# Optimization experiments

Hardware: AMD Instinct MI355X
Metric: run time of the kernel (lower is better)

Reference implementation:

```python
import jax, jax.numpy as jnp
import numpy as np

B, T = 8, 2048
DV, DA = 1024, 128          # visual / audio feature dims
D1, D2 = 512, 128           # conv1d channels
DH = D2 + DA + 1            # 257: lorentz dim after time-coord pad
DG = 128                    # per-branch GCN output dim (args.dim)
NEG = 0.01                  # LeakyReLU slope
K_CURV = 1.0
EPS = 1e-6


def leaky(x):
    return jnp.where(x >= 0, x, NEG * x)


def expmap0_lorentz(x):
    # x: [B,T,DH] with x[...,0] == 0 (tangent at origin), k = 1
    xs = x[..., 1:]
    n = jnp.sqrt(jnp.maximum(jnp.sum(xs * xs, -1, keepdims=True), 1e-12))
    return jnp.concatenate([jnp.cosh(n), jnp.sinh(n) / n * xs], axis=-1)


def lorentz_similarity(x):
    # xy_inner = -<x,x>_L  (negate time component of left factor, negate product)
    signs = jnp.concatenate([-jnp.ones((1,), x.dtype), jnp.ones((DH - 1,), x.dtype)])
    xy = -jnp.einsum('bid,bjd->bij', x * signs, x)          # [B,T,T]
    xy = jnp.maximum(xy, 1.0)                                # F.threshold(., 1, 1)
    d = (K_CURV ** 0.5) * jnp.log(xy + jnp.sqrt(xy * xy - 1.0 + 1e-7))
    return jnp.clip(d, EPS, 200.0)


def adj_fn(proj_x, seq_len):
    x2 = jnp.exp(-lorentz_similarity(proj_x))               # [B,T,T]
    pos = jnp.arange(T)
    row = pos[None, :, None] < seq_len[:, None, None]       # [B,T,1]
    col = pos[None, None, :] < seq_len[:, None, None]       # [B,1,T]
    thr = jnp.where(x2 > 0.8, x2, 0.0)                      # F.threshold(., 0.8, 0)
    logits = jnp.where(col, thr, -1e30)                     # softmax over valid cols
    p = jax.nn.softmax(logits, axis=-1)
    return p * (row & col)                                  # zero outside [:L,:L]


def clas_fn(logits, seq_len):
    # logits: [B,T]; per-sample top-k (k = L//16 + 1) mean, then sigmoid
    pos = jnp.arange(T)
    valid = pos[None, :] < seq_len[:, None]
    masked = jnp.where(valid, logits, -1e30)
    srt = -jnp.sort(-masked, axis=1)                         # descending
    k = seq_len // 16 + 1                                    # [B]
    kmask = pos[None, :] < k[:, None]
    mil = jnp.sum(srt * kmask, axis=1) / k.astype(logits.dtype)
    return jax.nn.sigmoid(mil)


def forward(inputs, seq_len, w1, b1, w2, b2, gw1, gw2, cls_w, cls_b):
    xv = inputs[:, :, :DV]
    xa = inputs[:, :, DV:]
    xv = leaky(jnp.einsum('btc,oc->bto', xv, w1) + b1)       # conv1d k=1
    xv = leaky(jnp.einsum('btc,oc->bto', xv, w2) + b2)
    x = jnp.concatenate([xv, xa], axis=-1)                   # [B,T,256]

    # DistanceAdj: exp(-|i-j| / e), shared across batch
    pos = jnp.arange(T, dtype=jnp.float32)
    disadj = jnp.exp(-jnp.abs(pos[:, None] - pos[None, :]) / jnp.exp(1.0))  # [T,T]

    # expm: pad time coord, lorentz expmap0
    proj_x = expmap0_lorentz(
        jnp.concatenate([jnp.zeros(x.shape[:-1] + (1,), x.dtype), x], axis=-1))  # [B,T,257]

    adj = adj_fn(proj_x, seq_len)                            # [B,T,T]

    x1 = leaky(jnp.einsum('bij,bjd->bid', adj, proj_x) @ gw1)        # HFSGCN stand-in
    x2 = leaky(jnp.einsum('ij,bjd->bid', disadj, proj_x) @ gw2)      # HTRGCN stand-in
    out_x = jnp.concatenate([x1, x2], axis=-1)               # [B,T,256]

    # HypClassifier: 2 + 2*<x, cls>_L + bias  (lorentz inner)
    signs = jnp.concatenate([-jnp.ones((1,), out_x.dtype), jnp.ones((2 * DG - 1,), out_x.dtype)])
    frame_prob = 2.0 + 2.0 * jnp.einsum('btd,cd->btc', out_x * signs, cls_w) + cls_b  # [B,T,1]

    mil_logits = clas_fn(frame_prob[..., 0], seq_len)        # [B]
    return mil_logits, frame_prob


def setup_inputs() -> dict:
    key = jax.random.key(0)
    ks = jax.random.split(key, 8)
    inputs = jax.random.normal(ks[0], (B, T, DV + DA), jnp.float32)
    seq_len = jax.random.randint(ks[1], (B,), T // 2, T + 1, jnp.int32)
    w1 = jax.random.normal(ks[2], (D1, DV), jnp.float32) / np.float32(np.sqrt(DV))
    b1 = jnp.zeros((D1,), jnp.float32)
    w2 = jax.random.normal(ks[3], (D2, D1), jnp.float32) / np.float32(np.sqrt(D1))
    b2 = jnp.zeros((D2,), jnp.float32)
    gw1 = jax.random.normal(ks[4], (DH, DG), jnp.float32) / np.float32(np.sqrt(DH))
    gw2 = jax.random.normal(ks[5], (DH, DG), jnp.float32) / np.float32(np.sqrt(DH))
    cls_w = jax.random.normal(ks[6], (1, 2 * DG), jnp.float32) / np.float32(np.sqrt(2 * DG))
    cls_b = jnp.zeros((1,), jnp.float32)
    return dict(inputs=inputs, seq_len=seq_len, w1=w1, b1=b1, w2=w2, b2=b2,
                gw1=gw1, gw2=gw2, cls_w=cls_w, cls_b=cls_b)


def reference(inputs, seq_len, w1, b1, w2, b2, gw1, gw2, cls_w, cls_b):
    return forward(inputs, seq_len, w1, b1, w2, b2, gw1, gw2, cls_w, cls_b)
```

## Files before the change

kernel.cpp:

```cpp
#include <hip/hip_runtime.h>
#include <math.h>

#define BB 8
#define TT 2048
#define DV_ 1024
#define DA_ 128
#define D1_ 512
#define D2_ 128
#define DH_ 257
#define DHP 288
#define DG_ 128
#define MTOT (BB*TT)
#define NPX ((size_t)MTOT*DHP)

#define NEGS 0.01f
#define INV_E 0.36787944117144233f
#define CH 64
#define HALO 64
#define UB 8

#define RS 40
#define BKC 32

static const size_t o_big = 0;
static const size_t o_c1  = 16777216;
static const size_t o_c2  = o_c1 + 8388608;
static const size_t o_w   = o_c2 + 2097152;
static const size_t o_S   = o_w + 663552;
static const size_t o_den = o_S + 2304;

static const size_t sw_w1h = 0;
static const size_t sw_w1l = 524288;
static const size_t sw_w2h = 1048576;
static const size_t sw_w2l = 1114112;
static const size_t sw_g1h = 1179648;
static const size_t sw_g1l = 1216512;
static const size_t sw_g2h = 1253376;
static const size_t sw_g2l = 1290240;

typedef __attribute__((ext_vector_type(8))) __bf16 bf16x8;
typedef __attribute__((ext_vector_type(8))) unsigned short us8;
typedef __attribute__((ext_vector_type(4))) float f32x4;

__device__ __forceinline__ float diag_w() {
    float dd = logf(1.0f + sqrtf(1.0f*1.0f - 1.0f + 1e-7f));
    dd = fminf(fmaxf(dd, 1e-6f), 200.0f);
    float x2 = expf(-dd);
    return expf(x2) - 1.0f;
}

__device__ __forceinline__ unsigned short f2bf(float f) {
    unsigned int u = __float_as_uint(f);
    u += 0x7FFFu + ((u >> 16) & 1u);
    return (unsigned short)(u >> 16);
}
__device__ __forceinline__ float bf2f(unsigned short h) {
    return __uint_as_float((unsigned int)h << 16);
}

__device__ __forceinline__ void cvt8(const float4 a, const float4 b,
                                     us8& h, us8& l) {
    unsigned short hh;
#define CV_(idx, val) hh = f2bf(val); h[idx] = hh; l[idx] = f2bf((val) - bf2f(hh));
    CV_(0, a.x) CV_(1, a.y) CV_(2, a.z) CV_(3, a.w)
    CV_(4, b.x) CV_(5, b.y) CV_(6, b.z) CV_(7, b.w)
#undef CV_
}

__global__ void k_setup(float* __restrict__ den, const int* __restrict__ seq,
                        float* __restrict__ S,
                        const float* __restrict__ w1, const float* __restrict__ w2,
                        unsigned short* __restrict__ h1, unsigned short* __restrict__ l1,
                        unsigned short* __restrict__ h2, unsigned short* __restrict__ l2,
                        const float* __restrict__ g1, const float* __restrict__ g2,
                        unsigned short* __restrict__ gh1, unsigned short* __restrict__ gl1,
                        unsigned short* __restrict__ gh2, unsigned short* __restrict__ gl2)
{
    const int bx = blockIdx.x;
    if (bx < 64) {
        int r = bx * 256 + threadIdx.x;
        den[r] = (float)seq[r >> 11] + diag_w();
        if (r < BB * DHP) S[r] = 0.f;
    } else if (bx < 640) {
        size_t i = ((size_t)(bx - 64) * 256 + threadIdx.x) * 4;
        const float* src; unsigned short *h, *l; size_t o;
        if (i < (size_t)D1_ * DV_) { src = w1; h = h1; l = l1; o = i; }
        else {
            o = i - (size_t)D1_ * DV_;
            if (o >= (size_t)D2_ * D1_) return;
            src = w2; h = h2; l = l2;
        }
        float4 v = *(const float4*)(src + o);
        ushort4 hv, lv;
        hv.x = f2bf(v.x); lv.x = f2bf(v.x - bf2f(hv.x));
        hv.y = f2bf(v.y); lv.y = f2bf(v.y - bf2f(hv.y));
        hv.z = f2bf(v.z); lv.z = f2bf(v.z - bf2f(hv.z));
        hv.w = f2bf(v.w); lv.w = f2bf(v.w - bf2f(hv.w));
        *(ushort4*)(h + o) = hv;
        *(ushort4*)(l + o) = lv;
    } else {
        const int bb = bx - 640;
        const int zz = (bb >= 144);
        int i = (bb - (zz ? 144 : 0)) * 256 + threadIdx.x;
        if (i >= DG_ * DHP) return;
        const float* g = zz ? g2 : g1;
        unsigned short* th = zz ? gh2 : gh1;
        unsigned short* tl = zz ? gl2 : gl1;
        int c = i / DHP, k = i - c * DHP;
        float v = (k < DH_) ? g[k * DG_ + c] : 0.f;
        unsigned short hh = f2bf(v);
        th[i] = hh;
        tl[i] = f2bf(v - bf2f(hh));
    }
}

__global__ __launch_bounds__(512, 2) void gemm_mlp1(
    const float* __restrict__ inA,
    const unsigned short* __restrict__ Bh, const unsigned short* __restrict__ Bl,
    const float* __restrict__ bias,
    unsigned short* __restrict__ Ch, unsigned short* __restrict__ Cl)
{
    __shared__ unsigned short sm[2][2][128 * RS];
    const int ib = blockIdx.x;
    const int x = ib & 7, slot = ib >> 3;
    const int cc = slot & 3, g = slot >> 2;
    const int row0 = (x + 8 * g) * 128, col0 = cc * 128;
    const int tid = threadIdx.x;
    const int wave = tid >> 6, lane = tid & 63;
    const int r0w = (wave >> 2) * 64;
    const int c0 = col0 + (wave & 3) * 32;
    const int q = lane >> 4, m = lane & 15;
    const int srow = tid >> 2, scol = (tid & 3) << 3;
    const size_t gA0 = (size_t)(row0 + srow) * 1152 + scol;
    const int s0 = srow * RS + scol;
    size_t bo_[2];
#pragma unroll
    for (int t = 0; t < 2; ++t) bo_[t] = (size_t)(c0 + t*16 + m) * DV_ + q*8;

    float4 a00, a01;
    bf16x8 fah[4], fal[4];
    bf16x8 bh0[2], bl0[2], bh1[2], bl1[2];

#define M1_LDGA(o) { \
    a00 = *(const float4*)(inA + gA0 + (o)); a01 = *(const float4*)(inA + gA0 + (o) + 4); }
#define M1_STAGE(BUF) { \
    us8 h_, l_; \
    cvt8(a00, a01, h_, l_); \
    *(us8*)&sm[BUF][0][s0] = h_; *(us8*)&sm[BUF][1][s0] = l_; }
#define M1_LDGB(S, o) \
    _Pragma("unroll") \
    for (int t = 0; t < 2; ++t) { \
        bh##S[t] = *(const bf16x8*)(Bh + bo_[t] + (o)); \
        bl##S[t] = *(const bf16x8*)(Bl + bo_[t] + (o)); }
#define M1_LOADA(BUF) \
    _Pragma("unroll") \
    for (int t = 0; t < 4; ++t) { \
        const int ra = (r0w + t*16 + m) * RS + q*8; \
        fah[t] = *(const bf16x8*)&sm[BUF][0][ra]; \
        fal[t] = *(const bf16x8*)&sm[BUF][1][ra]; }
#define M1_MFMA(S) \
    _Pragma("unroll") \
    for (int mi = 0; mi < 4; ++mi) \
        _Pragma("unroll") \
        for (int nj = 0; nj < 2; ++nj) { \
            acc[mi][nj] = __builtin_amdgcn_mfma_f32_16x16x32_bf16(fah[mi], bh##S[nj], acc[mi][nj], 0, 0, 0); \
            acc[mi][nj] = __builtin_amdgcn_mfma_f32_16x16x32_bf16(fal[mi], bh##S[nj], acc[mi][nj], 0, 0, 0); \
            acc[mi][nj] = __builtin_amdgcn_mfma_f32_16x16x32_bf16(fah[mi], bl##S[nj], acc[mi][nj], 0, 0, 0); \
        }

    f32x4 acc[4][2];
#pragma unroll
    for (int a = 0; a < 4; ++a)
#pragma unroll
        for (int c = 0; c < 2; ++c) acc[a][c] = (f32x4){0.f, 0.f, 0.f, 0.f};

    M1_LDGA(0)
    M1_STAGE(0)
    M1_LDGB(0, 0)
    __syncthreads();

    const int NI = (DV_ / BKC) / 2;
    for (int i = 0; i < NI; ++i) {
        const size_t o1 = (size_t)(2*i + 1) * BKC;
        M1_LDGA(o1)
        M1_LDGB(1, o1)
        M1_LOADA(0)
        M1_MFMA(0)
        M1_STAGE(1)
        __syncthreads();
        if (i + 1 < NI) {
            const size_t o2 = (size_t)(2*i + 2) * BKC;
            M1_LDGA(o2)
            M1_LDGB(0, o2)
        }
        M1_LOADA(1)
        M1_MFMA(1)
        if (i + 1 < NI) { M1_STAGE(0) }
        __syncthreads();
    }
#undef M1_LDGA
#undef M1_STAGE
#undef M1_LDGB
#undef M1_LOADA
#undef M1_MFMA

    float bj[2];
#pragma unroll
    for (int nj = 0; nj < 2; ++nj) bj[nj] = bias[c0 + nj*16 + m];
#pragma unroll
    for (int mi = 0; mi < 4; ++mi)
#pragma unroll
        for (int nj = 0; nj < 2; ++nj)
#pragma unroll
            for (int t = 0; t < 4; ++t) {
                int i = row0 + r0w + mi*16 + q*4 + t;
                int j = c0 + nj*16 + m;
                float v = acc[mi][nj][t] + bj[nj];
                v = (v >= 0.f) ? v : NEGS * v;
                size_t o = (size_t)i * D1_ + j;
                unsigned short hh = f2bf(v);
                Ch[o] = hh;
                Cl[o] = f2bf(v - bf2f(hh));
            }
}

#define LOADK(S, k0) \
    _Pragma("unroll") \
    for (int t = 0; t < 4; ++t) { \
        size_t ao = (size_t)(r0 + t*16 + m) * lda + (k0) + q*8; \
        size_t bo = (size_t)(c0 + t*16 + m) * ldb + (k0) + q*8; \
        ah##S[t] = *(const bf16x8*)(Ah + ao); \
        al##S[t] = *(const bf16x8*)(Al + ao); \
        bh##S[t] = *(const bf16x8*)(Bh + bo); \
        bl##S[t] = *(const bf16x8*)(Bl + bo); \
    }
#define MFMAK(S) \
    _Pragma("unroll") \
    for (int mi = 0; mi < 4; ++mi) \
        _Pragma("unroll") \
        for (int nj = 0; nj < 4; ++nj) { \
            acc[mi][nj] = __builtin_amdgcn_mfma_f32_16x16x32_bf16(ah##S[mi], bh##S[nj], acc[mi][nj], 0, 0, 0); \
            acc[mi][nj] = __builtin_amdgcn_mfma_f32_16x16x32_bf16(al##S[mi], bh##S[nj], acc[mi][nj], 0, 0, 0); \
            acc[mi][nj] = __builtin_amdgcn_mfma_f32_16x16x32_bf16(ah##S[mi], bl##S[nj], acc[mi][nj], 0, 0, 0); \
        }

#define LOADK2(S, k0, LD) \
    _Pragma("unroll") \
    for (int t = 0; t < 4; ++t) { \
        size_t ao = (size_t)(r0 + t*16 + m) * (LD) + (k0) + q*8; \
        ah##S[t] = *(const bf16x8*)(Ah + ao); \
        al##S[t] = *(const bf16x8*)(Al + ao); \
    } \
    _Pragma("unroll") \
    for (int t = 0; t < 2; ++t) { \
        size_t bo = (size_t)(c0 + t*16 + m) * (LD) + (k0) + q*8; \
        bh##S[t] = *(const bf16x8*)(Bh + bo); \
        bl##S[t] = *(const bf16x8*)(Bl + bo); \
    }
#define MFMAK2(S) \
    _Pragma("unroll") \
    for (int mi = 0; mi < 4; ++mi) \
        _Pragma("unroll") \
        for (int nj = 0; nj < 2; ++nj) { \
            acc[mi][nj] = __builtin_amdgcn_mfma_f32_16x16x32_bf16(ah##S[mi], bh##S[nj], acc[mi][nj], 0, 0, 0); \
            acc[mi][nj] = __builtin_amdgcn_mfma_f32_16x16x32_bf16(al##S[mi], bh##S[nj], acc[mi][nj], 0, 0, 0); \
            acc[mi][nj] = __builtin_amdgcn_mfma_f32_16x16x32_bf16(ah##S[mi], bl##S[nj], acc[mi][nj], 0, 0, 0); \
        }

__global__ __launch_bounds__(256, 1) void gemm_mlp2(
    const unsigned short* __restrict__ Ah, const unsigned short* __restrict__ Al,
    const unsigned short* __restrict__ Bh, const unsigned short* __restrict__ Bl,
    const float* __restrict__ bias, float* __restrict__ Cf)
{
    const int row0 = blockIdx.x * 64;
    const int wave = threadIdx.x >> 6, lane = threadIdx.x & 63;
    const int r0 = row0, c0 = wave * 32;
    const int q = lane >> 4, m = lane & 15;
    f32x4 acc[4][2];
#pragma unroll
    for (int a = 0; a < 4; ++a)
#pragma unroll
        for (int c = 0; c < 2; ++c) acc[a][c] = (f32x4){0.f, 0.f, 0.f, 0.f};
    bf16x8 ah0[4], al0[4], bh0[2], bl0[2];
    bf16x8 ah1[4], al1[4], bh1[2], bl1[2];
    LOADK2(0, 0, D1_)
    for (int k0 = 0; k0 + 64 <= D1_; k0 += 64) {
        LOADK2(1, k0 + 32, D1_)
        MFMAK2(0)
        if (k0 + 64 < D1_) { LOADK2(0, k0 + 64, D1_) }
        MFMAK2(1)
    }
    float bj[2];
#pragma unroll
    for (int nj = 0; nj < 2; ++nj) bj[nj] = bias[c0 + nj*16 + m];
#pragma unroll
    for (int mi = 0; mi < 4; ++mi)
#pragma unroll
        for (int nj = 0; nj < 2; ++nj)
#pragma unroll
            for (int t = 0; t < 4; ++t) {
                int i = r0 + mi*16 + q*4 + t;
                int j = c0 + nj*16 + m;
                float v = acc[mi][nj][t] + bj[nj];
                v = (v >= 0.f) ? v : NEGS * v;
                Cf[(size_t)i * D2_ + j] = v;
            }
}

__global__ __launch_bounds__(256, 1) void gemm_gc(
    const unsigned short* __restrict__ A1h, const unsigned short* __restrict__ A1l,
    const unsigned short* __restrict__ A2h, const unsigned short* __restrict__ A2l,
    const unsigned short* __restrict__ G1h, const unsigned short* __restrict__ G1l,
    const unsigned short* __restrict__ G2h, const unsigned short* __restrict__ G2l,
    float* __restrict__ X1, float* __restrict__ X2)
{
    const int z = blockIdx.z;
    const unsigned short* Ah = z ? A2h : A1h;
    const unsigned short* Al = z ? A2l : A1l;
    const unsigned short* Bh = z ? G2h : G1h;
    const unsigned short* Bl = z ? G2l : G1l;
    float* Cf = z ? X2 : X1;
    const int lda = DHP, ldb = DHP;
    const int row0 = blockIdx.y * 128, col0 = 0;
    const int wave = threadIdx.x >> 6, lane = threadIdx.x & 63;
    const int r0 = row0 + (wave >> 1) * 64, c0 = col0 + (wave & 1) * 64;
    const int q = lane >> 4, m = lane & 15;
    f32x4 acc[4][4];
#pragma unroll
    for (int a = 0; a < 4; ++a)
#pragma unroll
        for (int c = 0; c < 4; ++c) acc[a][c] = (f32x4){0.f, 0.f, 0.f, 0.f};
    bf16x8 ah0[4], al0[4], bh0[4], bl0[4];
    bf16x8 ah1[4], al1[4], bh1[4], bl1[4];
    LOADK(0, 0)
    int k0 = 0;
    for (; k0 + 64 <= DHP; k0 += 64) {
        LOADK(1, k0 + 32)
        MFMAK(0)
        if (k0 + 64 < DHP) { LOADK(0, k0 + 64) }
        MFMAK(1)
    }
    if (k0 < DHP) { MFMAK(0) }
#pragma unroll
    for (int mi = 0; mi < 4; ++mi)
#pragma unroll
        for (int nj = 0; nj < 4; ++nj)
#pragma unroll
            for (int t = 0; t < 4; ++t) {
                int i = r0 + mi*16 + q*4 + t;
                int j = c0 + nj*16 + m;
                float v = acc[mi][nj][t];
                v = (v >= 0.f) ? v : NEGS * v;
                Cf[(size_t)i * DG_ + j] = v;
            }
}

#define XLOAD(S, k0) \
    _Pragma("unroll") \
    for (int t = 0; t < 4; ++t) { \
        af##S[t] = *(const bf16x8*)(base + (size_t)(r0 + t*16 + m) * DHP + (k0) + q*8); \
        bf##S[t] = *(const bf16x8*)(base + (size_t)(c0 + t*16 + m) * DHP + (k0) + q*8); \
    }
#define XMFMA(S) \
    _Pragma("unroll") \
    for (int mi = 0; mi < 4; ++mi) \
        _Pragma("unroll") \
        for (int nj = 0; nj < 4; ++nj) \
            acc[mi][nj] = __builtin_amdgcn_mfma_f32_16x16x32_bf16(af##S[mi], bf##S[nj], acc[mi][nj], 0, 0, 0);

__global__ __launch_bounds__(256, 1) void k_mid(
    const unsigned short* __restrict__ pxb, const float* __restrict__ px,
    const int* __restrict__ seq, float* __restrict__ den,
    float* __restrict__ accb, float* __restrict__ S,
    unsigned short* __restrict__ yh, unsigned short* __restrict__ yl)
{
    __shared__ float Fs[CH][144];
    const int id = blockIdx.x;
    const int tid = threadIdx.x;

    if (id < 512) {
        const int t_ = id;
        const int zz = t_ >> 8;
        const int b = (t_ >> 5) & 7;
        const int i0 = (t_ & 31) * CH;
        const int d = zz * 144 + tid;
        const bool act = (tid < 144);
        const float r = expf(-INV_E);
        const float* base = px + (size_t)b * TT * DHP;
        if (act) {
            const int jlo = (i0 - HALO > 0) ? i0 - HALO : 0;
            float LA = 0.f;
            for (int j = jlo; j < i0 + CH; j += UB) {
                float va[UB];
#pragma unroll
                for (int u = 0; u < UB; ++u)
                    va[u] = base[(size_t)(j + u) * DHP + d];
#pragma unroll
                for (int u = 0; u < UB; ++u) {
                    LA = fmaf(r, LA, va[u]);
                    const int jj = j + u;
                    if (jj >= i0) Fs[jj - i0][tid] = LA;
                }
            }
            const int jhi = (i0 + CH - 1 + HALO < TT - 1) ? i0 + CH - 1 + HALO : TT - 1;
            float RA = 0.f;
            int j = jhi;
            for (; j >= i0 + CH; j -= UB) {
                float va[UB];
#pragma unroll
                for (int u = 0; u < UB; ++u)
                    va[u] = base[(size_t)(j - u) * DHP + d];
#pragma unroll
                for (int u = 0; u < UB; ++u) RA = fmaf(r, RA, va[u]);
            }
            for (; j >= i0; j -= UB) {
                float va[UB];
#pragma unroll
                for (int u = 0; u < UB; ++u)
                    va[u] = base[(size_t)(j - u) * DHP + d];
#pragma unroll
                for (int u = 0; u < UB; ++u) {
                    const int jj = j - u;
                    RA = fmaf(r, RA, va[u]);
                    size_t o = ((size_t)(b * TT + jj)) * DHP + d;
                    float ya = Fs[jj - i0][tid] + RA - va[u];
                    unsigned short hh = f2bf(ya);
                    yh[o] = hh; yl[o] = f2bf(ya - bf2f(hh));
                }
            }
        }
        return;
    }
    if (id < 1024) {
        const int t_ = id - 512;
        const int b = t_ >> 6, chunk = t_ & 63;
        const int nb = seq[b];
        const int j0 = chunk * 32;
        const int j1 = (j0 + 32 < nb) ? j0 + 32 : nb;
        float a0 = 0.f, a1 = 0.f;
        const bool hasB = (tid < DHP - 256);
        for (int j = j0; j < j1; ++j) {
            const float* row = px + ((size_t)(b * TT + j)) * DHP;
            a0 += row[tid];
            if (hasB) a1 += row[256 + tid];
        }
        if (j1 > j0) {
            atomicAdd(&S[b * DHP + tid], a0);
            if (hasB) atomicAdd(&S[b * DHP + 256 + tid], a1);
        }
        return;
    }
    {
        const int t_ = id - 1024;
        const int b = t_ >> 8;
        const int bx = t_ & 15, by = (t_ >> 4) & 15;
        if (bx < by) return;
        const int nb = seq[b];
        const int row0 = by * 128, col0 = bx * 128;
        if (row0 >= nb || col0 >= nb) return;
        const int wave = tid >> 6, lane = tid & 63;
        const int r0 = row0 + (wave >> 1) * 64, c0 = col0 + (wave & 1) * 64;
        if (c0 + 63 < r0 || r0 >= nb || c0 >= nb) return;
        const unsigned short* base = pxb + (size_t)b * TT * DHP;
        const int q = lane >> 4, m = lane & 15;
        f32x4 acc[4][4];
#pragma unroll
        for (int a = 0; a < 4; ++a)
#pragma unroll
            for (int c = 0; c < 4; ++c) acc[a][c] = (f32x4){0.f, 0.f, 0.f, 0.f};
        bf16x8 af0[4], bf0[4], af1[4], bf1[4];
        XLOAD(0, 0)
        int k0 = 0;
        for (; k0 + 64 <= DHP; k0 += 64) {
            XLOAD(1, k0 + 32)
            XMFMA(0)
            if (k0 + 64 < DHP) { XLOAD(0, k0 + 64) }
            XMFMA(1)
        }
        if (k0 < DHP) { XMFMA(0) }
        const float* b32 = px + (size_t)b * TT * DHP;
        float cj[4], ci[4][4];
#pragma unroll
        for (int nj = 0; nj < 4; ++nj) cj[nj] = b32[(size_t)(c0 + nj*16 + m) * DHP];
#pragma unroll
        for (int mi = 0; mi < 4; ++mi)
#pragma unroll
            for (int t = 0; t < 4; ++t) ci[mi][t] = b32[(size_t)(r0 + mi*16 + q*4 + t) * DHP];
#pragma unroll
        for (int mi = 0; mi < 4; ++mi)
#pragma unroll
            for (int nj = 0; nj < 4; ++nj)
#pragma unroll
                for (int t = 0; t < 4; ++t) {
                    int i = r0 + mi*16 + q*4 + t;
                    int j = c0 + nj*16 + m;
                    if (i < j && j < nb) {
                        float xyv = 2.f * ci[mi][t] * cj[nj] - acc[mi][nj][t];
                        float xym = fmaxf(xyv, 1.0f);
                        if (xym < 1.026f) {
                            float dd = logf(xym + sqrtf(xym * xym - 1.0f + 1e-7f));
                            dd = fminf(fmaxf(dd, 1e-6f), 200.0f);
                            float x2v = expf(-dd);
                            if (x2v > 0.8f) {
                                float w = expf(x2v) - 1.0f;
                                atomicAdd(&den[b * TT + i], w);
                                atomicAdd(&den[b * TT + j], w);
                                const float* pi = b32 + (size_t)i * DHP;
                                const float* pj = b32 + (size_t)j * DHP;
                                float* ai = accb + ((size_t)(b * TT + i)) * DHP;
                                float* aj = accb + ((size_t)(b * TT + j)) * DHP;
                                for (int d = 0; d < DHP; ++d) {
                                    atomicAdd(&ai[d], w * pj[d]);
                                    atomicAdd(&aj[d], w * pi[d]);
                                }
                            }
                        }
                    }
                }
    }
}

__global__ __launch_bounds__(256) void k_proj(
    const float* __restrict__ C2, const float* __restrict__ inputs,
    float* __restrict__ px, unsigned short* __restrict__ pxb,
    float* __restrict__ accb)
{
    const int r = blockIdx.x * 4 + (threadIdx.x >> 6);
    const int l = threadIdx.x & 63;
    float v[4];
#pragma unroll
    for (int e = 0; e < 2; ++e)
        v[e] = C2[(size_t)r * 128 + l + 64*e];
#pragma unroll
    for (int e = 2; e < 4; ++e)
        v[e] = inputs[(size_t)r * 1152 + 1024 + (l + 64*e - 128)];
    float sq = v[0]*v[0] + v[1]*v[1] + v[2]*v[2] + v[3]*v[3];
#pragma unroll
    for (int o = 32; o > 0; o >>= 1) sq += __shfl_xor(sq, o, 64);
    float n2 = fmaxf(sq, 1e-12f);
    float n = sqrtf(n2);
    float cs0 = coshf(n);
    float cs1 = sinhf(n) / n;
    const size_t base = (size_t)r * DHP;
#pragma unroll
    for (int e = 0; e < 4; ++e) {
        int idx = l + 64*e;
        float sv = cs1 * v[e];
        px[base + 1 + idx] = sv;
        pxb[base + 1 + idx] = f2bf(sv);
        accb[base + idx] = 0.f;
    }
    if (l == 0) { px[base] = cs0; pxb[base] = f2bf(cs0); }
    if (l < DHP - DH_) { px[base + DH_ + l] = 0.f; pxb[base + DH_ + l] = 0; }
    if (l < 32) accb[base + 256 + l] = 0.f;
}

__global__ void k_y1(const float* __restrict__ accb, const float* __restrict__ S,
                     const float* __restrict__ den, const int* __restrict__ seq,
                     const float* __restrict__ px,
                     unsigned short* __restrict__ yh, unsigned short* __restrict__ yl)
{
    size_t idx = (size_t)blockIdx.x * 256 + threadIdx.x;
    if (idx >= NPX) return;
    int r = (int)(idx / DHP);
    int b = r >> 11, i = r & (TT - 1);
    int d = (int)(idx - (size_t)r * DHP);
    float out = 0.f;
    if (i < seq[b])
        out = (S[b * DHP + d] + accb[idx] + diag_w() * px[idx]) / den[r];
    unsigned short hh = f2bf(out);
    yh[idx] = hh;
    yl[idx] = f2bf(out - bf2f(hh));
}

__global__ __launch_bounds__(256) void k_frame(
    const float* __restrict__ x1, const float* __restrict__ x2f,
    const float* __restrict__ cls_w, const float* __restrict__ cls_b,
    float* __restrict__ dout)
{
    const int r = blockIdx.x * 4 + (threadIdx.x >> 6);
    const int lane = threadIdx.x & 63;
    float s = 0.f;
#pragma unroll
    for (int t = 0; t < 2; ++t) {
        int g = lane + t * 64;
        float cw1 = cls_w[g];
        if (g == 0) cw1 = -cw1;
        s += x1[(size_t)r * DG_ + g] * cw1;
        s += x2f[(size_t)r * DG_ + g] * cls_w[DG_ + g];
    }
#pragma unroll
    for (int o = 32; o > 0; o >>= 1) s += __shfl_down(s, o, 64);
    if (lane == 0) dout[8 + r] = 2.0f + 2.0f * s + cls_b[0];
}

__global__ __launch_bounds__(1024) void k_clas(
    const int* __restrict__ seq, float* __restrict__ dout)
{
    __shared__ unsigned su[TT];
    __shared__ unsigned hist[256];
    __shared__ unsigned sh_prefix;
    __shared__ int sh_rem;
    __shared__ float wred[16];
    __shared__ int wcnt[16];
    const int b = blockIdx.x, tid = threadIdx.x;
    const int nb = seq[b];
    const int kk = nb / 16 + 1;
    for (int t = tid; t < TT; t += 1024) {
        unsigned u = 0u;
        if (t < nb) {
            unsigned x = __float_as_uint(dout[8 + b * TT + t]);
            u = (x & 0x80000000u) ? ~x : (x | 0x80000000u);
        }
        su[t] = u;
    }
    if (tid == 0) { sh_prefix = 0u; sh_rem = kk; }
    __syncthreads();
#pragma unroll
    for (int p = 0; p < 4; ++p) {
        const int shift = 24 - 8 * p;
        const unsigned hm = (p == 0) ? 0u : (0xFFFFFFFFu << (shift + 8));
        if (tid < 256) hist[tid] = 0u;
        __syncthreads();
        const unsigned pref = sh_prefix;
        for (int t = tid; t < TT; t += 1024) {
            unsigned u = su[t];
            if (u != 0u && (u & hm) == pref)
                atomicAdd(&hist[(u >> shift) & 0xFFu], 1u);
        }
        __syncthreads();
        if (tid == 0) {
            int rem = sh_rem;
            int v = 255;
            for (; v > 0; --v) {
                int c = (int)hist[v];
                if (c < rem) rem -= c;
                else break;
            }
            sh_rem = rem;
            sh_prefix = sh_prefix | ((unsigned)v << shift);
        }
        __syncthreads();
    }
    const unsigned T = sh_prefix;
    float fsum = 0.f; int cnt = 0;
    for (int t = tid; t < TT; t += 1024) {
        unsigned u = su[t];
        if (u > T) {
            unsigned x = (u & 0x80000000u) ? (u ^ 0x80000000u) : ~u;
            fsum += __uint_as_float(x);
            ++cnt;
        }
    }
#pragma unroll
    for (int o = 32; o > 0; o >>= 1) {
        fsum += __shfl_down(fsum, o, 64);
        cnt  += __shfl_down(cnt, o, 64);
    }
    if ((tid & 63) == 0) { wred[tid >> 6] = fsum; wcnt[tid >> 6] = cnt; }
    __syncthreads();
    if (tid == 0) {
        float s = 0.f; int c = 0;
#pragma unroll
        for (int t = 0; t < 16; ++t) { s += wred[t]; c += wcnt[t]; }
        unsigned x = (T & 0x80000000u) ? (T ^ 0x80000000u) : ~T;
        s += (float)(kk - c) * __uint_as_float(x);
        float mil = s / (float)kk;
        dout[b] = 1.f / (1.f + expf(-mil));
    }
}

extern "C" void kernel_launch(void* const* d_in, const int* in_sizes, int n_in,
                              void* d_out, int out_size, void* d_ws, size_t ws_size,
                              hipStream_t stream) {
    (void)in_sizes; (void)n_in; (void)out_size; (void)ws_size;
    const float* inputs = (const float*)d_in[0];
    const int*   seq    = (const int*)d_in[1];
    const float* w1     = (const float*)d_in[2];
    const float* b1     = (const float*)d_in[3];
    const float* w2     = (const float*)d_in[4];
    const float* b2     = (const float*)d_in[5];
    const float* gw1    = (const float*)d_in[6];
    const float* gw2    = (const float*)d_in[7];
    const float* cls_w  = (const float*)d_in[8];
    const float* cls_b  = (const float*)d_in[9];
    float* dout = (float*)d_out;
    float* ws = (float*)d_ws;

    float* px  = ws + o_big;
    unsigned short* pxb = (unsigned short*)(ws + o_big + 4718592);
    unsigned short* y2h = (unsigned short*)(ws + o_big + 7077888);
    unsigned short* y2l = y2h + NPX;
    unsigned short* y1h = (unsigned short*)(ws + o_big + 11796480);
    unsigned short* y1l = y1h + NPX;
    unsigned short* C1h = (unsigned short*)(ws + o_c1);
    unsigned short* C1l = C1h + (size_t)MTOT * D1_;
    float* accb = ws + o_c1;
    float* x1   = ws + o_c1 + 4718592;
    float* C2  = ws + o_c2;
    float* x2f = ws + o_c2;
    unsigned short* wsS = (unsigned short*)(ws + o_w);
    unsigned short *W1h = wsS + sw_w1h, *W1l = wsS + sw_w1l;
    unsigned short *W2h = wsS + sw_w2h, *W2l = wsS + sw_w2l;
    unsigned short *g1h = wsS + sw_g1h, *g1l = wsS + sw_g1l;
    unsigned short *g2h = wsS + sw_g2h, *g2l = wsS + sw_g2l;
    float* S   = ws + o_S;
    float* den = ws + o_den;

    k_setup<<<928, 256, 0, stream>>>(den, seq, S, w1, w2, W1h, W1l, W2h, W2l,
                                     gw1, gw2, g1h, g1l, g2h, g2l);

    gemm_mlp1<<<512, 512, 0, stream>>>(inputs, W1h, W1l, b1, C1h, C1l);
    gemm_mlp2<<<256, 256, 0, stream>>>(C1h, C1l, W2h, W2l, b2, C2);

    k_proj<<<MTOT / 4, 256, 0, stream>>>(C2, inputs, px, pxb, accb);

    k_mid<<<3072, 256, 0, stream>>>(pxb, px, seq, den, accb, S, y2h, y2l);

    k_y1<<<(int)(NPX / 256), 256, 0, stream>>>(accb, S, den, seq, px, y1h, y1l);

    gemm_gc<<<dim3(1, MTOT / 128, 2), 256, 0, stream>>>(
        y1h, y1l, y2h, y2l, g1h, g1l, g2h, g2l, x1, x2f);

    k_frame<<<MTOT / 4, 256, 0, stream>>>(x1, x2f, cls_w, cls_b, dout);
    k_clas<<<BB, 1024, 0, stream>>>(seq, dout);
}
```

Baseline: 372.5 us.

## Reorder k_mid block roles and fuse frame classifier into top-k kernel

Moves the heavy adjacency MFMA blocks to the lowest block indices in k_mid so they are dispatched first, with the scan and column-sum blocks filling in behind them. Removes the k_frame kernel and computes the frame logits inside k_clas, so the top-k selection uses them straight from registers without a launch and a round-trip through dout. In exchange, k_clas now runs only 8 blocks, each thread reading two 128-float rows per frame, which may make that stage slower to saturate bandwidth.

```diff
diff --git a/kernel.cpp b/kernel.cpp
--- a/kernel.cpp
+++ b/kernel.cpp
@@ -378,80 +378,8 @@
     const int id = blockIdx.x;
     const int tid = threadIdx.x;
 
-    if (id < 512) {
+    if (id < 2048) {
         const int t_ = id;
-        const int zz = t_ >> 8;
-        const int b = (t_ >> 5) & 7;
-        const int i0 = (t_ & 31) * CH;
-        const int d = zz * 144 + tid;
-        const bool act = (tid < 144);
-        const float r = expf(-INV_E);
-        const float* base = px + (size_t)b * TT * DHP;
-        if (act) {
-            const int jlo = (i0 - HALO > 0) ? i0 - HALO : 0;
-            float LA = 0.f;
-            for (int j = jlo; j < i0 + CH; j += UB) {
-                float va[UB];
-#pragma unroll
-                for (int u = 0; u < UB; ++u)
-                    va[u] = base[(size_t)(j + u) * DHP + d];
-#pragma unroll
-                for (int u = 0; u < UB; ++u) {
-                    LA = fmaf(r, LA, va[u]);
-                    const int jj = j + u;
-                    if (jj >= i0) Fs[jj - i0][tid] = LA;
-                }
-            }
-            const int jhi = (i0 + CH - 1 + HALO < TT - 1) ? i0 + CH - 1 + HALO : TT - 1;
-            float RA = 0.f;
-            int j = jhi;
-            for (; j >= i0 + CH; j -= UB) {
-                float va[UB];
-#pragma unroll
-                for (int u = 0; u < UB; ++u)
-                    va[u] = base[(size_t)(j - u) * DHP + d];
-#pragma unroll
-                for (int u = 0; u < UB; ++u) RA = fmaf(r, RA, va[u]);
-            }
-            for (; j >= i0; j -= UB) {
-                float va[UB];
-#pragma unroll
-                for (int u = 0; u < UB; ++u)
-                    va[u] = base[(size_t)(j - u) * DHP + d];
-#pragma unroll
-                for (int u = 0; u < UB; ++u) {
-                    const int jj = j - u;
-                    RA = fmaf(r, RA, va[u]);
-                    size_t o = ((size_t)(b * TT + jj)) * DHP + d;
-                    float ya = Fs[jj - i0][tid] + RA - va[u];
-                    unsigned short hh = f2bf(ya);
-                    yh[o] = hh; yl[o] = f2bf(ya - bf2f(hh));
-                }
-            }
-        }
-        return;
-    }
-    if (id < 1024) {
-        const int t_ = id - 512;
-        const int b = t_ >> 6, chunk = t_ & 63;
-        const int nb = seq[b];
-        const int j0 = chunk * 32;
-        const int j1 = (j0 + 32 < nb) ? j0 + 32 : nb;
-        float a0 = 0.f, a1 = 0.f;
-        const bool hasB = (tid < DHP - 256);
-        for (int j = j0; j < j1; ++j) {
-            const float* row = px + ((size_t)(b * TT + j)) * DHP;
-            a0 += row[tid];
-            if (hasB) a1 += row[256 + tid];
-        }
-        if (j1 > j0) {
-            atomicAdd(&S[b * DHP + tid], a0);
-            if (hasB) atomicAdd(&S[b * DHP + 256 + tid], a1);
-        }
-        return;
-    }
-    {
-        const int t_ = id - 1024;
         const int b = t_ >> 8;
         const int bx = t_ & 15, by = (t_ >> 4) & 15;
         if (bx < by) return;
@@ -517,6 +445,78 @@
                         }
                     }
                 }
+        return;
+    }
+    if (id < 2560) {
+        const int t_ = id - 2048;
+        const int zz = t_ >> 8;
+        const int b = (t_ >> 5) & 7;
+        const int i0 = (t_ & 31) * CH;
+        const int d = zz * 144 + tid;
+        const bool act = (tid < 144);
+        const float r = expf(-INV_E);
+        const float* base = px + (size_t)b * TT * DHP;
+        if (act) {
+            const int jlo = (i0 - HALO > 0) ? i0 - HALO : 0;
+            float LA = 0.f;
+            for (int j = jlo; j < i0 + CH; j += UB) {
+                float va[UB];
+#pragma unroll
+                for (int u = 0; u < UB; ++u)
+                    va[u] = base[(size_t)(j + u) * DHP + d];
+#pragma unroll
+                for (int u = 0; u < UB; ++u) {
+                    LA = fmaf(r, LA, va[u]);
+                    const int jj = j + u;
+                    if (jj >= i0) Fs[jj - i0][tid] = LA;
+                }
+            }
+            const int jhi = (i0 + CH - 1 + HALO < TT - 1) ? i0 + CH - 1 + HALO : TT - 1;
+            float RA = 0.f;
+            int j = jhi;
+            for (; j >= i0 + CH; j -= UB) {
+                float va[UB];
+#pragma unroll
+                for (int u = 0; u < UB; ++u)
+                    va[u] = base[(size_t)(j - u) * DHP + d];
+#pragma unroll
+                for (int u = 0; u < UB; ++u) RA = fmaf(r, RA, va[u]);
+            }
+            for (; j >= i0; j -= UB) {
+                float va[UB];
+#pragma unroll
+                for (int u = 0; u < UB; ++u)
+                    va[u] = base[(size_t)(j - u) * DHP + d];
+#pragma unroll
+                for (int u = 0; u < UB; ++u) {
+                    const int jj = j - u;
+                    RA = fmaf(r, RA, va[u]);
+                    size_t o = ((size_t)(b * TT + jj)) * DHP + d;
+                    float ya = Fs[jj - i0][tid] + RA - va[u];
+                    unsigned short hh = f2bf(ya);
+                    yh[o] = hh; yl[o] = f2bf(ya - bf2f(hh));
+                }
+            }
+        }
+        return;
+    }
+    {
+        const int t_ = id - 2560;
+        const int b = t_ >> 6, chunk = t_ & 63;
+        const int nb = seq[b];
+        const int j0 = chunk * 32;
+        const int j1 = (j0 + 32 < nb) ? j0 + 32 : nb;
+        float a0 = 0.f, a1 = 0.f;
+        const bool hasB = (tid < DHP - 256);
+        for (int j = j0; j < j1; ++j) {
+            const float* row = px + ((size_t)(b * TT + j)) * DHP;
+            a0 += row[tid];
+            if (hasB) a1 += row[256 + tid];
+        }
+        if (j1 > j0) {
+            atomicAdd(&S[b * DHP + tid], a0);
+            if (hasB) atomicAdd(&S[b * DHP + 256 + tid], a1);
+        }
     }
 }
 
@@ -573,28 +573,9 @@
     yl[idx] = f2bf(out - bf2f(hh));
 }
 
-__global__ __launch_bounds__(256) void k_frame(
+__global__ __launch_bounds__(1024) void k_clas(
     const float* __restrict__ x1, const float* __restrict__ x2f,
     const float* __restrict__ cls_w, const float* __restrict__ cls_b,
-    float* __restrict__ dout)
-{
-    const int r = blockIdx.x * 4 + (threadIdx.x >> 6);
-    const int lane = threadIdx.x & 63;
-    float s = 0.f;
-#pragma unroll
-    for (int t = 0; t < 2; ++t) {
-        int g = lane + t * 64;
-        float cw1 = cls_w[g];
-        if (g == 0) cw1 = -cw1;
-        s += x1[(size_t)r * DG_ + g] * cw1;
-        s += x2f[(size_t)r * DG_ + g] * cls_w[DG_ + g];
-    }
-#pragma unroll
-    for (int o = 32; o > 0; o >>= 1) s += __shfl_down(s, o, 64);
-    if (lane == 0) dout[8 + r] = 2.0f + 2.0f * s + cls_b[0];
-}
-
-__global__ __launch_bounds__(1024) void k_clas(
     const int* __restrict__ seq, float* __restrict__ dout)
 {
     __shared__ unsigned su[TT];
@@ -606,10 +587,30 @@
     const int b = blockIdx.x, tid = threadIdx.x;
     const int nb = seq[b];
     const int kk = nb / 16 + 1;
+    const float cb = cls_b[0];
     for (int t = tid; t < TT; t += 1024) {
+        const int r = b * TT + t;
+        const float* xr = x1  + (size_t)r * DG_;
+        const float* yr = x2f + (size_t)r * DG_;
+        float s = 0.f;
+#pragma unroll 4
+        for (int j = 0; j < DG_; j += 4) {
+            float4 a = *(const float4*)(xr + j);
+            float4 w = *(const float4*)(cls_w + j);
+            s += a.x*w.x + a.y*w.y + a.z*w.z + a.w*w.w;
+        }
+        s -= 2.f * xr[0] * cls_w[0];
+#pragma unroll 4
+        for (int j = 0; j < DG_; j += 4) {
+            float4 a = *(const float4*)(yr + j);
+            float4 w = *(const float4*)(cls_w + DG_ + j);
+            s += a.x*w.x + a.y*w.y + a.z*w.z + a.w*w.w;
+        }
+        float fp = 2.0f + 2.0f * s + cb;
+        dout[8 + r] = fp;
         unsigned u = 0u;
         if (t < nb) {
-            unsigned x = __float_as_uint(dout[8 + b * TT + t]);
+            unsigned x = __float_as_uint(fp);
             u = (x & 0x80000000u) ? ~x : (x | 0x80000000u);
         }
         su[t] = u;
@@ -722,6 +723,5 @@
     gemm_gc<<<dim3(1, MTOT / 128, 2), 256, 0, stream>>>(
         y1h, y1l, y2h, y2l, g1h, g1l, g2h, g2l, x1, x2f);
 
-    k_frame<<<MTOT / 4, 256, 0, stream>>>(x1, x2f, cls_w, cls_b, dout);
-    k_clas<<<BB, 1024, 0, stream>>>(seq, dout);
-}
+    k_clas<<<BB, 1024, 0, stream>>>(x1, x2f, cls_w, cls_b, seq, dout);
+}
```

After: 430.9 us. 15.7% more time.
